# Performance work log

Hardware: AMD Instinct MI355X
Metric: run time of the kernel (lower is better)

Reference implementation:

```python
import jax, jax.numpy as jnp
import numpy as np

N = 30000          # num nodes
E = 480000         # num edges (before self-loops)
D_MODEL = 128
HEADS = 8
HEAD_DIM = D_MODEL // HEADS  # 16
LAYERS = 7
NUM_LABELS = 2
NEG_SLOPE = 0.2


def setup_inputs() -> dict:
    key = jax.random.key(0)
    ks = jax.random.split(key, 10)
    s = 0.05
    x = jax.random.normal(ks[0], (N, D_MODEL), dtype=jnp.float32)
    edge_index = jax.random.randint(ks[1], (2, E), 0, N, dtype=jnp.int64)
    Wl = jax.random.normal(ks[2], (LAYERS, D_MODEL, D_MODEL), dtype=jnp.float32) * s
    bl = jnp.zeros((LAYERS, D_MODEL), dtype=jnp.float32)
    Wr = jax.random.normal(ks[3], (LAYERS, D_MODEL, D_MODEL), dtype=jnp.float32) * s
    br = jnp.zeros((LAYERS, D_MODEL), dtype=jnp.float32)
    att = jax.random.normal(ks[4], (LAYERS, HEADS, HEAD_DIM), dtype=jnp.float32) * s
    bias = jnp.zeros((LAYERS, D_MODEL), dtype=jnp.float32)
    W_out = jax.random.normal(ks[5], (D_MODEL, 1), dtype=jnp.float32) * s
    b_out = jnp.zeros((1,), dtype=jnp.float32)
    return {"x": x, "edge_index": edge_index, "Wl": Wl, "bl": bl,
            "Wr": Wr, "br": br, "att": att, "bias": bias,
            "W_out": W_out, "b_out": b_out}


def _gatv2_layer(x, Wl, bl, Wr, br, att, bias, src, dst):
    # x: [N, d]; src/dst: [E'] (with self-loops). GATv2 (dropout off / eval).
    xl = (x @ Wl + bl).reshape(N, HEADS, HEAD_DIM)  # source transform
    xr = (x @ Wr + br).reshape(N, HEADS, HEAD_DIM)  # target transform
    m = xl[src] + xr[dst]                           # [E', H, D]
    e = jnp.einsum('ehd,hd->eh', jax.nn.leaky_relu(m, NEG_SLOPE), att)  # [E', H]
    # segment softmax over destination nodes (self-loops => no empty segments)
    emax = jax.ops.segment_max(e, dst, num_segments=N)  # [N, H]
    ee = jnp.exp(e - emax[dst])
    denom = jax.ops.segment_sum(ee, dst, num_segments=N)  # [N, H]
    alpha = ee / (denom[dst] + 1e-16)                      # [E', H]
    out = jax.ops.segment_sum(alpha[:, :, None] * xl[src], dst, num_segments=N)
    return out.reshape(N, D_MODEL) + bias


def reference(x, edge_index, Wl, bl, Wr, br, att, bias, W_out, b_out):
    loops = jnp.arange(N, dtype=edge_index.dtype)
    src = jnp.concatenate([edge_index[0], loops])  # add_self_loops=True (PyG default)
    dst = jnp.concatenate([edge_index[1], loops])
    for i in range(LAYERS):
        x = _gatv2_layer(x, Wl[i], bl[i], Wr[i], br[i], att[i], bias[i], src, dst)
    y = x @ W_out + b_out            # [N, 1]
    return y[:NUM_LABELS, 0].reshape(1, -1)  # [1, num_labels]
```

## Files before the change

kernel.cpp:

```cpp
#include <hip/hip_runtime.h>
#include <hip/hip_fp16.h>

#define NN 30000
#define ER 480000
#define ET 510000
#define D 128
#define NH 8
#define HD 16
#define NL 7
#define SLOPE 0.2f
#define NB_SCAN 118

typedef unsigned int uint32;
typedef unsigned short ushort;
typedef __attribute__((ext_vector_type(8))) short short8;
typedef __attribute__((ext_vector_type(4))) float f32x4;
typedef _Float16 h2_t __attribute__((ext_vector_type(2)));

#if defined(__has_builtin)
#if __has_builtin(__builtin_amdgcn_fdot2)
#define HAS_FDOT2 1
#endif
#endif

__device__ inline ushort f2bf(float f) {
    uint32 u = __float_as_uint(f);
    return (ushort)((u + 0x7fffu + ((u >> 16) & 1u)) >> 16);
}
__device__ inline float bf2f(ushort h) {
    return __uint_as_float(((uint32)h) << 16);
}

__device__ inline __half2 hmax2p(__half2 a, __half2 b) {
    h2_t x = *reinterpret_cast<h2_t*>(&a), y = *reinterpret_cast<h2_t*>(&b);
    h2_t r;
    r[0] = x[0] > y[0] ? x[0] : y[0];
    r[1] = x[1] > y[1] ? x[1] : y[1];
    return *reinterpret_cast<__half2*>(&r);
}
__device__ inline __half2 hmin2p(__half2 a, __half2 b) {
    h2_t x = *reinterpret_cast<h2_t*>(&a), y = *reinterpret_cast<h2_t*>(&b);
    h2_t r;
    r[0] = x[0] < y[0] ? x[0] : y[0];
    r[1] = x[1] < y[1] ? x[1] : y[1];
    return *reinterpret_cast<__half2*>(&r);
}

__device__ inline float score_dot(__half2 l2, __half2 a2, float acc) {
#ifdef HAS_FDOT2
    h2_t x = *reinterpret_cast<h2_t*>(&l2);
    h2_t a = *reinterpret_cast<h2_t*>(&a2);
    return __builtin_amdgcn_fdot2(x, a, acc, false);
#else
    float2 lf = __half22float2(l2);
    float2 af = __half22float2(a2);
    return fmaf(lf.x, af.x, fmaf(lf.y, af.y, acc));
#endif
}


__global__ void k_zero(int* __restrict__ p, int n) {
    int i = blockIdx.x * 256 + threadIdx.x;
    if (i < n) p[i] = 0;
}

__global__ void k_hist(const int* __restrict__ ei, int* __restrict__ counts) {
    int i = blockIdx.x * 256 + threadIdx.x;
    if (i >= ET) return;
    int dst = (i < ER) ? ei[ER + i] : (i - ER);
    atomicAdd(&counts[dst], 1);
}

__global__ __launch_bounds__(256) void k_scan1(const int* __restrict__ counts,
                                               int* __restrict__ offsets,
                                               int* __restrict__ partials) {
    int t = threadIdx.x;
    int i = blockIdx.x * 256 + t;
    int v = (i < NN) ? counts[i] : 0;
    int lane = t & 63;
    int incl = v;
#pragma unroll
    for (int d = 1; d < 64; d <<= 1) {
        int u = __shfl_up(incl, d);
        if (lane >= d) incl += u;
    }
    __shared__ int ws[4];
    if (lane == 63) ws[t >> 6] = incl;
    __syncthreads();
    int wid = t >> 6;
    int base = 0;
    if (wid > 0) base += ws[0];
    if (wid > 1) base += ws[1];
    if (wid > 2) base += ws[2];
    if (i < NN) offsets[i] = base + incl - v;
    if (t == 255) partials[blockIdx.x] = base + incl;
}

__global__ __launch_bounds__(128) void k_scan2(int* __restrict__ partials,
                                               int* __restrict__ offsets) {
    int t = threadIdx.x;
    int v = (t < NB_SCAN) ? partials[t] : 0;
    int lane = t & 63;
    int incl = v;
#pragma unroll
    for (int d = 1; d < 64; d <<= 1) {
        int u = __shfl_up(incl, d);
        if (lane >= d) incl += u;
    }
    __shared__ int w0;
    if (t == 63) w0 = incl;
    __syncthreads();
    int base = (t >= 64) ? w0 : 0;
    if (t < NB_SCAN) partials[t] = base + incl - v;
    if (t == 127) offsets[NN] = base + incl;
}

__global__ void k_scan3(const int* __restrict__ partials, int* __restrict__ offsets,
                        int* __restrict__ cursor) {
    int i = blockIdx.x * 256 + threadIdx.x;
    if (i < NN) {
        int o = offsets[i] + partials[blockIdx.x];
        offsets[i] = o;
        cursor[i] = o;
    }
}

__global__ void k_scatter(const int* __restrict__ ei, int* __restrict__ cursor,
                          int* __restrict__ srcs) {
    int i = blockIdx.x * 256 + threadIdx.x;
    if (i >= ET) return;
    int src, dst;
    if (i < ER) { src = ei[i]; dst = ei[ER + i]; }
    else        { src = i - ER; dst = src; }
    int pos = atomicAdd(&cursor[dst], 1);
    srcs[pos] = src;
}


__global__ __launch_bounds__(256) void k_wprep(const float* __restrict__ Wl,
                                               const float* __restrict__ Wr,
                                               ushort* __restrict__ Wth,
                                               ushort* __restrict__ Wtl) {
    int bx = blockIdx.x;
    int layer = bx >> 3;
    int n0 = (bx & 7) * 32;
    const float* WL = Wl + (size_t)layer * D * D;
    const float* WR = Wr + (size_t)layer * D * D;
    ushort* th = Wth + (size_t)layer * 256 * 128;
    ushort* tl = Wtl + (size_t)layer * 256 * 128;
    for (int idx = threadIdx.x; idx < 32 * 128; idx += 256) {
        int n = n0 + (idx >> 7);
        int k = idx & 127;
        float w = (n < 128) ? WL[k * 128 + n] : WR[k * 128 + (n - 128)];
        ushort h = f2bf(w);
        ushort e = f2bf(w - bf2f(h));
        th[n * 128 + k] = h;
        tl[n * 128 + k] = e;
    }
}


__global__ void k_xsplit(const float* __restrict__ x,
                         ushort* __restrict__ xh, ushort* __restrict__ xe) {
    int i = (blockIdx.x * 256 + threadIdx.x) * 4;
    if (i >= NN * D) return;
    float4 f = *reinterpret_cast<const float4*>(x + i);
    ushort4 h, e;
    h.x = f2bf(f.x); e.x = f2bf(f.x - bf2f(h.x));
    h.y = f2bf(f.y); e.y = f2bf(f.y - bf2f(h.y));
    h.z = f2bf(f.z); e.z = f2bf(f.z - bf2f(h.z));
    h.w = f2bf(f.w); e.w = f2bf(f.w - bf2f(h.w));
    *reinterpret_cast<ushort4*>(xh + i) = h;
    *reinterpret_cast<ushort4*>(xe + i) = e;
}


__global__ __launch_bounds__(256) void k_mm(const ushort* __restrict__ Xh,
                                            const ushort* __restrict__ Xe,
                                            const ushort* __restrict__ Wth,
                                            const ushort* __restrict__ Wtl,
                                            const float* __restrict__ bl,
                                            const float* __restrict__ br,
                                            ushort* __restrict__ xlh,
                                            ushort* __restrict__ xrh) {
    __shared__ ushort Wh[64][136];
    __shared__ ushort We[64][136];
    const int row0 = blockIdx.x * 64;
    const int nq = blockIdx.y;
    const int tid = threadIdx.x;
    const int wv = tid >> 6;
    const int l  = tid & 63;
    const int lr = l & 15;
    const int kg = (l >> 4) * 8;

    {
        int nn = tid >> 2;
        int ch = tid & 3;
        const ushort* wh = Wth + (size_t)(nq * 64 + nn) * 128;
        const ushort* wl = Wtl + (size_t)(nq * 64 + nn) * 128;
#pragma unroll
        for (int pass = 0; pass < 4; ++pass) {
            int ko = (ch * 4 + pass) * 8;
            *reinterpret_cast<uint4*>(&Wh[nn][ko]) = *reinterpret_cast<const uint4*>(wh + ko);
            *reinterpret_cast<uint4*>(&We[nn][ko]) = *reinterpret_cast<const uint4*>(wl + ko);
        }
    }
    short8 Ah[4], Ae[4];
    {
        int row = row0 + wv * 16 + lr; if (row >= NN) row = NN - 1;
        const ushort* xh = Xh + (size_t)row * D;
        const ushort* xe = Xe + (size_t)row * D;
#pragma unroll
        for (int kc = 0; kc < 4; ++kc) {
            Ah[kc] = *reinterpret_cast<const short8*>(xh + kc * 32 + kg);
            Ae[kc] = *reinterpret_cast<const short8*>(xe + kc * 32 + kg);
        }
    }
    __syncthreads();

    f32x4 acc[4] = {};
#pragma unroll
    for (int kc = 0; kc < 4; ++kc) {
#pragma unroll
        for (int nc = 0; nc < 4; ++nc) {
            short8 Bh = *reinterpret_cast<const short8*>(&Wh[nc * 16 + lr][kc * 32 + kg]);
            short8 Be = *reinterpret_cast<const short8*>(&We[nc * 16 + lr][kc * 32 + kg]);
            acc[nc] = __builtin_amdgcn_mfma_f32_16x16x32_bf16(Ah[kc], Bh, acc[nc], 0, 0, 0);
            acc[nc] = __builtin_amdgcn_mfma_f32_16x16x32_bf16(Ah[kc], Be, acc[nc], 0, 0, 0);
            acc[nc] = __builtin_amdgcn_mfma_f32_16x16x32_bf16(Ae[kc], Bh, acc[nc], 0, 0, 0);
        }
    }
    const int rbase = row0 + wv * 16 + (l >> 4) * 4;
#pragma unroll
    for (int nc = 0; nc < 4; ++nc) {
        int g = nq * 64 + nc * 16 + lr;
        float bb = (g < 128) ? bl[g] : br[g - 128];
        ushort* dst = (g < 128) ? (xlh + g) : (xrh + (g - 128));
#pragma unroll
        for (int j = 0; j < 4; ++j) {
            int row = rbase + j;
            if (row < NN)
                dst[(size_t)row * D] = __half_as_ushort(__float2half_rn(acc[nc][j] + bb));
        }
    }
}


#define PROC(v)                                                                 \
    {                                                                           \
        __half2 vh0 = *reinterpret_cast<const __half2*>(&(v).x);                \
        __half2 vh1 = *reinterpret_cast<const __half2*>(&(v).y);                \
        __half2 t0 = __hadd2(vh0, rh0);                                         \
        __half2 t1 = __hadd2(vh1, rh1);                                         \
        __half2 l0 = __hfma2(hmin2p(t0, zero2), slope2, hmax2p(t0, zero2));     \
        __half2 l1 = __hfma2(hmin2p(t1, zero2), slope2, hmax2p(t1, zero2));     \
        float e = score_dot(l0, a0, score_dot(l1, a1, 0.f));                    \
        e += __shfl_xor(e, 1);                                                  \
        e += __shfl_xor(e, 2);                                                  \
        float p = __expf(e);                                                    \
        float2 f0 = __half22float2(vh0);                                        \
        float2 f1 = __half22float2(vh1);                                        \
        s += p;                                                                 \
        acc0 = fmaf(p, f0.x, acc0);                                             \
        acc1 = fmaf(p, f0.y, acc1);                                             \
        acc2 = fmaf(p, f1.x, acc2);                                             \
        acc3 = fmaf(p, f1.y, acc3);                                             \
    }

__global__ __launch_bounds__(256) void k_fused(const int* __restrict__ offsets,
                                               const int* __restrict__ srcs,
                                               const uint32* __restrict__ xlh,
                                               const uint32* __restrict__ xrh,
                                               const float* __restrict__ att,
                                               const float* __restrict__ bias,
                                               uint32* __restrict__ outH,
                                               uint32* __restrict__ outE) {
    const int tid = threadIdx.x;
    const int lane = tid & 63;
    const int half = lane >> 5;
    const int sl = lane & 31;
    const int n = blockIdx.x * 4 + (tid >> 6);
    const int off = offsets[n];
    const int deg = offsets[n + 1] - off;

    uint2 ru = *reinterpret_cast<const uint2*>(&xrh[(size_t)n * 64 + 2 * sl]);
    const __half2 rh0 = *reinterpret_cast<const __half2*>(&ru.x);
    const __half2 rh1 = *reinterpret_cast<const __half2*>(&ru.y);
    float4 af = *reinterpret_cast<const float4*>(&att[4 * sl]);
    const __half2 a0 = __floats2half2_rn(af.x, af.y);
    const __half2 a1 = __floats2half2_rn(af.z, af.w);
    const __half2 zero2 = __float2half2_rn(0.f);
    const __half2 slope2 = __float2half2_rn(SLOPE);

    float s = 0.f, acc0 = 0.f, acc1 = 0.f, acc2 = 0.f, acc3 = 0.f;

    int i = half;
    for (; i + 6 < deg; i += 8) {
        int s0 = srcs[off + i];
        int s1 = srcs[off + i + 2];
        int s2 = srcs[off + i + 4];
        int s3 = srcs[off + i + 6];
        uint2 v0 = *reinterpret_cast<const uint2*>(&xlh[(size_t)s0 * 64 + 2 * sl]);
        uint2 v1 = *reinterpret_cast<const uint2*>(&xlh[(size_t)s1 * 64 + 2 * sl]);
        uint2 v2 = *reinterpret_cast<const uint2*>(&xlh[(size_t)s2 * 64 + 2 * sl]);
        uint2 v3 = *reinterpret_cast<const uint2*>(&xlh[(size_t)s3 * 64 + 2 * sl]);
        PROC(v0); PROC(v1); PROC(v2); PROC(v3);
    }
    for (; i < deg; i += 2) {
        int sid = srcs[off + i];
        uint2 v = *reinterpret_cast<const uint2*>(&xlh[(size_t)sid * 64 + 2 * sl]);
        PROC(v);
    }

    s += __shfl_xor(s, 32);
    acc0 += __shfl_xor(acc0, 32);
    acc1 += __shfl_xor(acc1, 32);
    acc2 += __shfl_xor(acc2, 32);
    acc3 += __shfl_xor(acc3, 32);

    if (half == 0) {
        float inv = 1.f / (s + 1e-16f);
        float4 bb = *reinterpret_cast<const float4*>(&bias[4 * sl]);
        float o0 = acc0 * inv + bb.x;
        float o1 = acc1 * inv + bb.y;
        float o2 = acc2 * inv + bb.z;
        float o3 = acc3 * inv + bb.w;
        ushort h0 = f2bf(o0), h1 = f2bf(o1), h2 = f2bf(o2), h3 = f2bf(o3);
        ushort e0 = f2bf(o0 - bf2f(h0)), e1 = f2bf(o1 - bf2f(h1));
        ushort e2 = f2bf(o2 - bf2f(h2)), e3 = f2bf(o3 - bf2f(h3));
        uint2 wh, we;
        wh.x = (uint32)h0 | ((uint32)h1 << 16);
        wh.y = (uint32)h2 | ((uint32)h3 << 16);
        we.x = (uint32)e0 | ((uint32)e1 << 16);
        we.y = (uint32)e2 | ((uint32)e3 << 16);
        *reinterpret_cast<uint2*>(&outH[(size_t)n * 64 + 2 * sl]) = wh;
        *reinterpret_cast<uint2*>(&outE[(size_t)n * 64 + 2 * sl]) = we;
    }
}


__global__ void k_out(const ushort* __restrict__ xh, const ushort* __restrict__ xe,
                      const float* __restrict__ Wout, const float* __restrict__ bout,
                      float* __restrict__ y) {
    int lane = threadIdx.x;
#pragma unroll
    for (int i = 0; i < 2; ++i) {
        float x0 = bf2f(xh[i * D + lane]) + bf2f(xe[i * D + lane]);
        float x1 = bf2f(xh[i * D + 64 + lane]) + bf2f(xe[i * D + 64 + lane]);
        float v = x0 * Wout[lane] + x1 * Wout[64 + lane];
        v += __shfl_xor(v, 1); v += __shfl_xor(v, 2); v += __shfl_xor(v, 4);
        v += __shfl_xor(v, 8); v += __shfl_xor(v, 16); v += __shfl_xor(v, 32);
        if (lane == 0) y[i] = v + bout[0];
    }
}


extern "C" void kernel_launch(void* const* d_in, const int* in_sizes, int n_in,
                              void* d_out, int out_size, void* d_ws, size_t ws_size,
                              hipStream_t stream) {
    const float* x_in = (const float*)d_in[0];
    const int*   ei   = (const int*)d_in[1];
    const float* Wl   = (const float*)d_in[2];
    const float* bl   = (const float*)d_in[3];
    const float* Wr   = (const float*)d_in[4];
    const float* br   = (const float*)d_in[5];
    const float* att  = (const float*)d_in[6];
    const float* bias = (const float*)d_in[7];
    const float* Wout = (const float*)d_in[8];
    const float* bout = (const float*)d_in[9];
    float* y = (float*)d_out;

    char* ws = (char*)d_ws;
    size_t o = 0;
    auto alloc = [&](size_t bytes) -> void* {
        void* p = ws + o;
        o = (o + bytes + 255) & ~(size_t)255;
        return p;
    };
    ushort* XhA = (ushort*)alloc((size_t)NN * D * 2);
    ushort* XeA = (ushort*)alloc((size_t)NN * D * 2);
    ushort* XhB = (ushort*)alloc((size_t)NN * D * 2);
    ushort* XeB = (ushort*)alloc((size_t)NN * D * 2);
    ushort* xlh = (ushort*)alloc((size_t)NN * D * 2);
    ushort* xrh = (ushort*)alloc((size_t)NN * D * 2);
    ushort* Wth = (ushort*)alloc((size_t)NL * 256 * 128 * 2);
    ushort* Wtl = (ushort*)alloc((size_t)NL * 256 * 128 * 2);
    int* counts   = (int*)alloc((size_t)NN * 4);
    int* offsets  = (int*)alloc(((size_t)NN + 1) * 4);
    int* cursor   = (int*)alloc((size_t)NN * 4);
    int* srcs     = (int*)alloc((size_t)ET * 4);
    int* partials = (int*)alloc(256 * 4);
    (void)ws_size; (void)in_sizes; (void)n_in; (void)out_size;

    k_zero<<<NB_SCAN, 256, 0, stream>>>(counts, NN);
    k_hist<<<(ET + 255) / 256, 256, 0, stream>>>(ei, counts);
    k_scan1<<<NB_SCAN, 256, 0, stream>>>(counts, offsets, partials);
    k_scan2<<<1, 128, 0, stream>>>(partials, offsets);
    k_scan3<<<NB_SCAN, 256, 0, stream>>>(partials, offsets, cursor);
    k_scatter<<<(ET + 255) / 256, 256, 0, stream>>>(ei, cursor, srcs);
    k_wprep<<<NL * 8, 256, 0, stream>>>(Wl, Wr, Wth, Wtl);
    k_xsplit<<<NN * D / 1024, 256, 0, stream>>>(x_in, XhA, XeA);

    const int mgrid = (NN + 63) / 64;
    for (int i = 0; i < NL; ++i) {
        const ushort* inH = (i & 1) ? XhB : XhA;
        const ushort* inE = (i & 1) ? XeB : XeA;
        ushort* oH = (i & 1) ? XhA : XhB;
        ushort* oE = (i & 1) ? XeA : XeB;
        k_mm<<<dim3(mgrid, 4), 256, 0, stream>>>(inH, inE,
                                                 Wth + (size_t)i * 256 * 128,
                                                 Wtl + (size_t)i * 256 * 128,
                                                 bl + i * D, br + i * D, xlh, xrh);
        k_fused<<<NN / 4, 256, 0, stream>>>(offsets, srcs, (const uint32*)xlh,
                                            (const uint32*)xrh,
                                            att + i * NH * HD, bias + i * D,
                                            (uint32*)oH, (uint32*)oE);
    }
    k_out<<<1, 64, 0, stream>>>(XhB, XeB, Wout, bout, y);
}
```

Before: 392.5 us.

## Process four edges per wave with 16-byte gathers and read weights directly

The aggregation kernel now splits each 64-lane wave into four 16-lane groups. Each lane handles 8 features with 16-byte loads, so four edges are gathered at once instead of two, and the score reduction needs one shuffle instead of two. Tail edges are masked with a validity flag. Separately, the matmul kernel drops its shared-memory staging and barrier for the weight tiles and loads B fragments straight from global memory (likely L2/L1 resident). The risks are more per-lane register pressure, extra cross-group reduction shuffles at the end, and redundant global weight reads across waves.

```diff
diff --git a/kernel.cpp b/kernel.cpp
--- a/kernel.cpp
+++ b/kernel.cpp
@@ -183,8 +183,6 @@
                                             const float* __restrict__ br,
                                             ushort* __restrict__ xlh,
                                             ushort* __restrict__ xrh) {
-    __shared__ ushort Wh[64][136];
-    __shared__ ushort We[64][136];
     const int row0 = blockIdx.x * 64;
     const int nq = blockIdx.y;
     const int tid = threadIdx.x;
@@ -193,18 +191,6 @@
     const int lr = l & 15;
     const int kg = (l >> 4) * 8;
 
-    {
-        int nn = tid >> 2;
-        int ch = tid & 3;
-        const ushort* wh = Wth + (size_t)(nq * 64 + nn) * 128;
-        const ushort* wl = Wtl + (size_t)(nq * 64 + nn) * 128;
-#pragma unroll
-        for (int pass = 0; pass < 4; ++pass) {
-            int ko = (ch * 4 + pass) * 8;
-            *reinterpret_cast<uint4*>(&Wh[nn][ko]) = *reinterpret_cast<const uint4*>(wh + ko);
-            *reinterpret_cast<uint4*>(&We[nn][ko]) = *reinterpret_cast<const uint4*>(wl + ko);
-        }
-    }
     short8 Ah[4], Ae[4];
     {
         int row = row0 + wv * 16 + lr; if (row >= NN) row = NN - 1;
@@ -216,15 +202,15 @@
             Ae[kc] = *reinterpret_cast<const short8*>(xe + kc * 32 + kg);
         }
     }
-    __syncthreads();
 
     f32x4 acc[4] = {};
 #pragma unroll
     for (int kc = 0; kc < 4; ++kc) {
 #pragma unroll
         for (int nc = 0; nc < 4; ++nc) {
-            short8 Bh = *reinterpret_cast<const short8*>(&Wh[nc * 16 + lr][kc * 32 + kg]);
-            short8 Be = *reinterpret_cast<const short8*>(&We[nc * 16 + lr][kc * 32 + kg]);
+            size_t wo = (size_t)(nq * 64 + nc * 16 + lr) * 128 + kc * 32 + kg;
+            short8 Bh = *reinterpret_cast<const short8*>(Wth + wo);
+            short8 Be = *reinterpret_cast<const short8*>(Wtl + wo);
             acc[nc] = __builtin_amdgcn_mfma_f32_16x16x32_bf16(Ah[kc], Bh, acc[nc], 0, 0, 0);
             acc[nc] = __builtin_amdgcn_mfma_f32_16x16x32_bf16(Ah[kc], Be, acc[nc], 0, 0, 0);
             acc[nc] = __builtin_amdgcn_mfma_f32_16x16x32_bf16(Ae[kc], Bh, acc[nc], 0, 0, 0);
@@ -246,25 +232,35 @@
 }
 
 
-#define PROC(v)                                                                 \
+#define PROC(v, valid)                                                          \
     {                                                                           \
         __half2 vh0 = *reinterpret_cast<const __half2*>(&(v).x);                \
         __half2 vh1 = *reinterpret_cast<const __half2*>(&(v).y);                \
+        __half2 vh2 = *reinterpret_cast<const __half2*>(&(v).z);                \
+        __half2 vh3 = *reinterpret_cast<const __half2*>(&(v).w);                \
         __half2 t0 = __hadd2(vh0, rh0);                                         \
         __half2 t1 = __hadd2(vh1, rh1);                                         \
+        __half2 t2 = __hadd2(vh2, rh2);                                         \
+        __half2 t3 = __hadd2(vh3, rh3);                                         \
         __half2 l0 = __hfma2(hmin2p(t0, zero2), slope2, hmax2p(t0, zero2));     \
         __half2 l1 = __hfma2(hmin2p(t1, zero2), slope2, hmax2p(t1, zero2));     \
-        float e = score_dot(l0, a0, score_dot(l1, a1, 0.f));                    \
+        __half2 l2 = __hfma2(hmin2p(t2, zero2), slope2, hmax2p(t2, zero2));     \
+        __half2 l3 = __hfma2(hmin2p(t3, zero2), slope2, hmax2p(t3, zero2));     \
+        float e = score_dot(l0, a0,                                             \
+                  score_dot(l1, a1,                                             \
+                  score_dot(l2, a2,                                             \
+                  score_dot(l3, a3, 0.f))));                                    \
         e += __shfl_xor(e, 1);                                                  \
-        e += __shfl_xor(e, 2);                                                  \
-        float p = __expf(e);                                                    \
+        float p = (valid) ? __expf(e) : 0.f;                                    \
         float2 f0 = __half22float2(vh0);                                        \
         float2 f1 = __half22float2(vh1);                                        \
+        float2 f2 = __half22float2(vh2);                                        \
+        float2 f3 = __half22float2(vh3);                                        \
         s += p;                                                                 \
-        acc0 = fmaf(p, f0.x, acc0);                                             \
-        acc1 = fmaf(p, f0.y, acc1);                                             \
-        acc2 = fmaf(p, f1.x, acc2);                                             \
-        acc3 = fmaf(p, f1.y, acc3);                                             \
+        ac0 = fmaf(p, f0.x, ac0); ac1 = fmaf(p, f0.y, ac1);                     \
+        ac2 = fmaf(p, f1.x, ac2); ac3 = fmaf(p, f1.y, ac3);                     \
+        ac4 = fmaf(p, f2.x, ac4); ac5 = fmaf(p, f2.y, ac5);                     \
+        ac6 = fmaf(p, f3.x, ac6); ac7 = fmaf(p, f3.y, ac7);                     \
     }
 
 __global__ __launch_bounds__(256) void k_fused(const int* __restrict__ offsets,
@@ -277,64 +273,78 @@
                                                uint32* __restrict__ outE) {
     const int tid = threadIdx.x;
     const int lane = tid & 63;
-    const int half = lane >> 5;
-    const int sl = lane & 31;
+    const int q = lane >> 4;
+    const int sl = lane & 15;
     const int n = blockIdx.x * 4 + (tid >> 6);
     const int off = offsets[n];
     const int deg = offsets[n + 1] - off;
 
-    uint2 ru = *reinterpret_cast<const uint2*>(&xrh[(size_t)n * 64 + 2 * sl]);
+    uint4 ru = *reinterpret_cast<const uint4*>(&xrh[(size_t)n * 64 + 4 * sl]);
     const __half2 rh0 = *reinterpret_cast<const __half2*>(&ru.x);
     const __half2 rh1 = *reinterpret_cast<const __half2*>(&ru.y);
-    float4 af = *reinterpret_cast<const float4*>(&att[4 * sl]);
-    const __half2 a0 = __floats2half2_rn(af.x, af.y);
-    const __half2 a1 = __floats2half2_rn(af.z, af.w);
+    const __half2 rh2 = *reinterpret_cast<const __half2*>(&ru.z);
+    const __half2 rh3 = *reinterpret_cast<const __half2*>(&ru.w);
+    float4 af0 = *reinterpret_cast<const float4*>(&att[8 * sl]);
+    float4 af1 = *reinterpret_cast<const float4*>(&att[8 * sl + 4]);
+    const __half2 a0 = __floats2half2_rn(af0.x, af0.y);
+    const __half2 a1 = __floats2half2_rn(af0.z, af0.w);
+    const __half2 a2 = __floats2half2_rn(af1.x, af1.y);
+    const __half2 a3 = __floats2half2_rn(af1.z, af1.w);
     const __half2 zero2 = __float2half2_rn(0.f);
     const __half2 slope2 = __float2half2_rn(SLOPE);
 
-    float s = 0.f, acc0 = 0.f, acc1 = 0.f, acc2 = 0.f, acc3 = 0.f;
-
-    int i = half;
-    for (; i + 6 < deg; i += 8) {
-        int s0 = srcs[off + i];
-        int s1 = srcs[off + i + 2];
-        int s2 = srcs[off + i + 4];
-        int s3 = srcs[off + i + 6];
-        uint2 v0 = *reinterpret_cast<const uint2*>(&xlh[(size_t)s0 * 64 + 2 * sl]);
-        uint2 v1 = *reinterpret_cast<const uint2*>(&xlh[(size_t)s1 * 64 + 2 * sl]);
-        uint2 v2 = *reinterpret_cast<const uint2*>(&xlh[(size_t)s2 * 64 + 2 * sl]);
-        uint2 v3 = *reinterpret_cast<const uint2*>(&xlh[(size_t)s3 * 64 + 2 * sl]);
-        PROC(v0); PROC(v1); PROC(v2); PROC(v3);
-    }
-    for (; i < deg; i += 2) {
-        int sid = srcs[off + i];
-        uint2 v = *reinterpret_cast<const uint2*>(&xlh[(size_t)sid * 64 + 2 * sl]);
-        PROC(v);
-    }
-
-    s += __shfl_xor(s, 32);
-    acc0 += __shfl_xor(acc0, 32);
-    acc1 += __shfl_xor(acc1, 32);
-    acc2 += __shfl_xor(acc2, 32);
-    acc3 += __shfl_xor(acc3, 32);
-
-    if (half == 0) {
+    float s = 0.f;
+    float ac0 = 0.f, ac1 = 0.f, ac2 = 0.f, ac3 = 0.f;
+    float ac4 = 0.f, ac5 = 0.f, ac6 = 0.f, ac7 = 0.f;
+
+    int base = 0;
+    for (; base + 8 <= deg; base += 8) {
+        int s0 = srcs[off + base + q];
+        int s1 = srcs[off + base + 4 + q];
+        uint4 v0 = *reinterpret_cast<const uint4*>(&xlh[(size_t)s0 * 64 + 4 * sl]);
+        uint4 v1 = *reinterpret_cast<const uint4*>(&xlh[(size_t)s1 * 64 + 4 * sl]);
+        PROC(v0, true);
+        PROC(v1, true);
+    }
+    for (; base < deg; base += 4) {
+        int idx = base + q;
+        bool valid = idx < deg;
+        int sid = srcs[off + (valid ? idx : deg - 1)];
+        uint4 v = *reinterpret_cast<const uint4*>(&xlh[(size_t)sid * 64 + 4 * sl]);
+        PROC(v, valid);
+    }
+
+    s += __shfl_xor(s, 16);  s += __shfl_xor(s, 32);
+    ac0 += __shfl_xor(ac0, 16); ac0 += __shfl_xor(ac0, 32);
+    ac1 += __shfl_xor(ac1, 16); ac1 += __shfl_xor(ac1, 32);
+    ac2 += __shfl_xor(ac2, 16); ac2 += __shfl_xor(ac2, 32);
+    ac3 += __shfl_xor(ac3, 16); ac3 += __shfl_xor(ac3, 32);
+    ac4 += __shfl_xor(ac4, 16); ac4 += __shfl_xor(ac4, 32);
+    ac5 += __shfl_xor(ac5, 16); ac5 += __shfl_xor(ac5, 32);
+    ac6 += __shfl_xor(ac6, 16); ac6 += __shfl_xor(ac6, 32);
+    ac7 += __shfl_xor(ac7, 16); ac7 += __shfl_xor(ac7, 32);
+
+    if (q == 0) {
         float inv = 1.f / (s + 1e-16f);
-        float4 bb = *reinterpret_cast<const float4*>(&bias[4 * sl]);
-        float o0 = acc0 * inv + bb.x;
-        float o1 = acc1 * inv + bb.y;
-        float o2 = acc2 * inv + bb.z;
-        float o3 = acc3 * inv + bb.w;
+        float4 b0 = *reinterpret_cast<const float4*>(&bias[8 * sl]);
+        float4 b1 = *reinterpret_cast<const float4*>(&bias[8 * sl + 4]);
+        float o0 = ac0 * inv + b0.x, o1 = ac1 * inv + b0.y;
+        float o2 = ac2 * inv + b0.z, o3 = ac3 * inv + b0.w;
+        float o4 = ac4 * inv + b1.x, o5 = ac5 * inv + b1.y;
+        float o6 = ac6 * inv + b1.z, o7 = ac7 * inv + b1.w;
         ushort h0 = f2bf(o0), h1 = f2bf(o1), h2 = f2bf(o2), h3 = f2bf(o3);
-        ushort e0 = f2bf(o0 - bf2f(h0)), e1 = f2bf(o1 - bf2f(h1));
-        ushort e2 = f2bf(o2 - bf2f(h2)), e3 = f2bf(o3 - bf2f(h3));
-        uint2 wh, we;
+        ushort h4 = f2bf(o4), h5 = f2bf(o5), h6 = f2bf(o6), h7 = f2bf(o7);
+        uint4 wh, we;
         wh.x = (uint32)h0 | ((uint32)h1 << 16);
         wh.y = (uint32)h2 | ((uint32)h3 << 16);
-        we.x = (uint32)e0 | ((uint32)e1 << 16);
-        we.y = (uint32)e2 | ((uint32)e3 << 16);
-        *reinterpret_cast<uint2*>(&outH[(size_t)n * 64 + 2 * sl]) = wh;
-        *reinterpret_cast<uint2*>(&outE[(size_t)n * 64 + 2 * sl]) = we;
+        wh.z = (uint32)h4 | ((uint32)h5 << 16);
+        wh.w = (uint32)h6 | ((uint32)h7 << 16);
+        we.x = (uint32)f2bf(o0 - bf2f(h0)) | ((uint32)f2bf(o1 - bf2f(h1)) << 16);
+        we.y = (uint32)f2bf(o2 - bf2f(h2)) | ((uint32)f2bf(o3 - bf2f(h3)) << 16);
+        we.z = (uint32)f2bf(o4 - bf2f(h4)) | ((uint32)f2bf(o5 - bf2f(h5)) << 16);
+        we.w = (uint32)f2bf(o6 - bf2f(h6)) | ((uint32)f2bf(o7 - bf2f(h7)) << 16);
+        *reinterpret_cast<uint4*>(&outH[(size_t)n * 64 + 4 * sl]) = wh;
+        *reinterpret_cast<uint4*>(&outE[(size_t)n * 64 + 4 * sl]) = we;
     }
 }
 
```

New measurement: 529.8 us. 35.0% more time.
